# Optimization experiments

Measured on AMD Instinct MI355X. Metric: run time of the kernel, lower is better.

Reference implementation:

```python
import jax, jax.numpy as jnp
import numpy as np


def conv2d(x, w, b, pad):
    # x: [B,Cin,H,W], w: [Cout,Cin,kh,kw]
    y = jax.lax.conv_general_dilated(
        x, w, window_strides=(1, 1), padding=[(pad, pad), (pad, pad)],
        dimension_numbers=('NCHW', 'OIHW', 'NCHW'))
    return y + b[None, :, None, None]


def setup_inputs() -> dict:
    key = jax.random.key(0)
    ks = jax.random.split(key, 11)
    B, C, H, W = 4, 128, 64, 64
    Cc, Hc, Wc = 256, 32, 32
    s = 0.05
    return {
        'sr_feat': jax.random.normal(ks[0], (B, C, H, W), jnp.float32),
        'context_feat': jax.random.normal(ks[1], (B, Cc, Hc, Wc), jnp.float32),
        'Wq': jax.random.normal(ks[2], (C, C, 1, 1), jnp.float32) * s,
        'bq': jax.random.normal(ks[3], (C,), jnp.float32) * s,
        'Wk': jax.random.normal(ks[4], (C, Cc, 1, 1), jnp.float32) * s,
        'bk': jax.random.normal(ks[5], (C,), jnp.float32) * s,
        'Wv': jax.random.normal(ks[6], (C, Cc, 1, 1), jnp.float32) * s,
        'bv': jax.random.normal(ks[7], (C,), jnp.float32) * s,
        'Wp': jax.random.normal(ks[8], (C, C, 3, 3), jnp.float32) * s,
        'bp': jax.random.normal(ks[9], (C,), jnp.float32) * s,
        'gamma': jax.random.normal(ks[10], (1,), jnp.float32) * s,
    }


def reference(sr_feat, context_feat, Wq, bq, Wk, bk, Wv, bv, Wp, bp, gamma):
    B, C, H, W = sr_feat.shape
    Cc = context_feat.shape[1]
    # bilinear upsample (half-pixel centers == align_corners=False)
    ctx = jax.image.resize(context_feat, (B, Cc, H, W), method='bilinear')
    q = conv2d(sr_feat, Wq, bq, 0).reshape(B, C, H * W)   # [B,C,N]
    k = conv2d(ctx, Wk, bk, 0).reshape(B, C, H * W)       # [B,C,N]
    v = conv2d(ctx, Wv, bv, 0).reshape(B, C, H * W)       # [B,C,N]
    # attn[b,n,m] = softmax_m( sum_c q[b,c,n] * k[b,c,m] )
    attn = jax.nn.softmax(jnp.einsum('bcn,bcm->bnm', q, k), axis=-1)
    # out[b,c,n] = sum_m v[b,c,m] * attn[b,n,m]
    out = jnp.einsum('bcm,bnm->bcn', v, attn).reshape(B, C, H, W)
    return sr_feat + gamma[0] * conv2d(out, Wp, bp, 1)
```

## Files before the change

### kernel.cpp

```cpp
#include <hip/hip_runtime.h>
#include <math.h>

#define NB 4
#define C  128
#define CCH 256
#define HH 64
#define WW 64
#define NN 4096
#define HC 32
#define WC 32
#define PP 66
#define LOG2E 1.44269504088896f
#define NSPLIT 4

typedef unsigned short u16;
typedef unsigned int uint32;
typedef short s16x8 __attribute__((ext_vector_type(8)));
typedef float f32x4 __attribute__((ext_vector_type(4)));
typedef float f32x16 __attribute__((ext_vector_type(16)));

#if __has_builtin(__builtin_amdgcn_exp2f)
#define EXP2(x) __builtin_amdgcn_exp2f(x)
#else
#define EXP2(x) __expf((x) * 0.69314718056f)
#endif

__device__ __forceinline__ u16 f2bf(float f) {
    uint32 u = __float_as_uint(f);
    u += 0x7fffu + ((u >> 16) & 1u);
    return (u16)(u >> 16);
}
__device__ __forceinline__ float bf2f(u16 h) {
    return __uint_as_float((uint32)h << 16);
}

__global__ __launch_bounds__(256) void prep_all(const float* __restrict__ ctx,
                                                const float* __restrict__ sr,
                                                const float* __restrict__ Wq,
                                                const float* __restrict__ Wk,
                                                const float* __restrict__ Wv,
                                                const float* __restrict__ Wp,
                                                u16* __restrict__ ctx_t,
                                                u16* __restrict__ sr_t,
                                                u16* __restrict__ wbf,
                                                u16* __restrict__ wt,
                                                uint4* __restrict__ att_z) {
    __shared__ float smem[2 * 32 * 130];
    int blk = blockIdx.x;
    int tid = threadIdx.x;

    if (blk < 512) {
        float (*ls)[32][130] = (float(*)[32][130])smem;
        int y = blk & 63;
        int cch = (blk >> 6) & 1;
        int b = blk >> 7;
        float sy = y * 0.5f - 0.25f;
        int y0 = (int)floorf(sy);
        float wy = sy - (float)y0;
        int y0c = y0 < 0 ? 0 : y0;
        int y1c = (y0 + 1 > HC - 1) ? HC - 1 : y0 + 1;
#pragma unroll
        for (int t = 0; t < 4; t++) {
            int CI = t * 256 + tid;
            int cc = CI >> 3, xq = CI & 7;
            const float* s = ctx + (size_t)(b * CCH + cch * 128 + cc) * (HC * WC);
            float4 v0 = *(const float4*)(s + y0c * WC + xq * 4);
            float4 v1 = *(const float4*)(s + y1c * WC + xq * 4);
            ls[0][xq * 4 + 0][cc] = v0.x; ls[0][xq * 4 + 1][cc] = v0.y;
            ls[0][xq * 4 + 2][cc] = v0.z; ls[0][xq * 4 + 3][cc] = v0.w;
            ls[1][xq * 4 + 0][cc] = v1.x; ls[1][xq * 4 + 1][cc] = v1.y;
            ls[1][xq * 4 + 2][cc] = v1.z; ls[1][xq * 4 + 3][cc] = v1.w;
        }
        __syncthreads();
        int occ = tid & 127, xh = tid >> 7;
        u16* ob = ctx_t + ((size_t)b * NN + (size_t)y * 64) * CCH + cch * 128 + occ;
        float wy1 = 1.f - wy;
#pragma unroll
        for (int xi = 0; xi < 32; xi++) {
            int x = xi * 2 + xh;
            float sx = x * 0.5f - 0.25f;
            int x0 = (int)floorf(sx);
            float wx = sx - (float)x0;
            int x0c = x0 < 0 ? 0 : x0;
            int x1c = (x0 + 1 > WC - 1) ? WC - 1 : x0 + 1;
            float v00 = ls[0][x0c][occ], v01 = ls[0][x1c][occ];
            float v10 = ls[1][x0c][occ], v11 = ls[1][x1c][occ];
            float val = wy1 * ((1.f - wx) * v00 + wx * v01)
                      + wy  * ((1.f - wx) * v10 + wx * v11);
            ob[(size_t)x * CCH] = f2bf(val);
        }
    } else if (blk < 1024) {
        float* ls = smem;
        int idx = blk - 512;
        int n0 = (idx & 63) * 64;
        int ci0 = ((idx >> 6) & 1) * 64;
        int b = idx >> 7;
        const float* inb = sr + ((size_t)b * C + ci0) * NN + n0;
#pragma unroll
        for (int L = 0; L < 4; L++) {
            int fc = tid + L * 256;
            int nc = fc & 15, ci = fc >> 4;
            float4 v = *(const float4*)(inb + (size_t)ci * NN + nc * 4);
            float* d = &ls[ci * 65 + nc * 4];
            d[0] = v.x; d[1] = v.y; d[2] = v.z; d[3] = v.w;
        }
        __syncthreads();
        u16* ob = sr_t + ((size_t)b * NN + n0) * C + ci0;
#pragma unroll
        for (int j = 0; j < 16; j++) {
            int o = tid + j * 256;
            int ci = o & 63, n = o >> 6;
            ob[(size_t)n * C + ci] = f2bf(ls[ci * 65 + n]);
        }
    } else if (blk < 1920) {
        int i = (blk - 1024) * 256 + tid;
        if (i < 81920) {
            float v;
            if (i < 16384) v = Wq[i] * LOG2E;
            else if (i < 49152) v = Wk[i - 16384];
            else v = Wv[i - 49152];
            wbf[i] = f2bf(v);
        } else {
            int idx = i - 81920;
            int ciin = idx & 31;
            int co = (idx >> 5) & 127;
            int cb = (idx >> 12) & 3;
            int pos = idx >> 14;
            int ky = pos / 3, kx = pos - ky * 3;
            int ci = cb * 32 + ciin;
            wt[idx] = f2bf(Wp[((size_t)(co * C + ci) * 3 + ky) * 3 + kx]);
        }
    } else {
        int i = (blk - 1920) * 256 + tid;
        if (i < 278784) att_z[i] = make_uint4(0, 0, 0, 0);
    }
}

__global__ __launch_bounds__(256) void proj_all(const u16* __restrict__ sr_t,
                                                const u16* __restrict__ ctx_t,
                                                const u16* __restrict__ wbf,
                                                const float* __restrict__ bq,
                                                const float* __restrict__ bk,
                                                const float* __restrict__ bv,
                                                u16* __restrict__ q_t,
                                                u16* __restrict__ k_t,
                                                u16* __restrict__ v_bf) {
    __shared__ u16 xs[128 * 64];
    __shared__ u16 wsm[128 * 64];
    int z = blockIdx.z;
    int b = blockIdx.y;
    int n0 = blockIdx.x * 128;
    int Cin = (z == 0) ? C : CCH;
    const u16* xb = (z == 0 ? sr_t : ctx_t) + (size_t)b * NN * Cin;
    const u16* wb = wbf + (z == 0 ? 0 : (z == 1 ? 16384 : 49152));
    const float* bias = (z == 0) ? bq : (z == 1 ? bk : bv);
    float bsc = (z == 0) ? LOG2E : 1.0f;
    bool vmode = (z == 2);

    int tid = threadIdx.x;
    int w = tid >> 6, lane = tid & 63, l31 = lane & 31, half = lane >> 5;
    int xh = w >> 1, wh = w & 1;

    f32x16 acc[2][2];
#pragma unroll
    for (int xt = 0; xt < 2; xt++)
#pragma unroll
        for (int wt2 = 0; wt2 < 2; wt2++)
#pragma unroll
            for (int i = 0; i < 16; i++) acc[xt][wt2][i] = 0.f;

    int nchunks = Cin >> 6;
    for (int c0i = 0; c0i < nchunks; c0i++) {
        int c0 = c0i * 64;
        __syncthreads();
#pragma unroll
        for (int t = 0; t < 4; t++) {
            int CI = t * 256 + tid;
            int row = CI >> 3, sl = CI & 7;
            int lc = sl ^ (row & 7);
            __builtin_amdgcn_global_load_lds(
                (const __attribute__((address_space(1))) void*)(xb + (size_t)(n0 + row) * Cin + c0 + lc * 8),
                (__attribute__((address_space(3))) void*)&xs[(size_t)CI * 8], 16, 0, 0);
        }
#pragma unroll
        for (int t = 0; t < 4; t++) {
            int CI = t * 256 + tid;
            int co = CI >> 3, sl = CI & 7;
            int lc = sl ^ (co & 7);
            __builtin_amdgcn_global_load_lds(
                (const __attribute__((address_space(1))) void*)(wb + (size_t)co * Cin + c0 + lc * 8),
                (__attribute__((address_space(3))) void*)&wsm[(size_t)CI * 8], 16, 0, 0);
        }
        __syncthreads();
#pragma unroll
        for (int kg = 0; kg < 4; kg++) {
            int pc = ((kg * 2 + half) ^ (l31 & 7)) * 8;
            s16x8 xf[2], wf2[2];
#pragma unroll
            for (int xt = 0; xt < 2; xt++)
                xf[xt] = *(const s16x8*)&xs[(xh * 64 + xt * 32 + l31) * 64 + pc];
#pragma unroll
            for (int wt2 = 0; wt2 < 2; wt2++)
                wf2[wt2] = *(const s16x8*)&wsm[(wh * 64 + wt2 * 32 + l31) * 64 + pc];
#pragma unroll
            for (int xt = 0; xt < 2; xt++)
#pragma unroll
                for (int wt2 = 0; wt2 < 2; wt2++) {
                    if (vmode)
                        acc[xt][wt2] = __builtin_amdgcn_mfma_f32_32x32x16_bf16(wf2[wt2], xf[xt], acc[xt][wt2], 0, 0, 0);
                    else
                        acc[xt][wt2] = __builtin_amdgcn_mfma_f32_32x32x16_bf16(xf[xt], wf2[wt2], acc[xt][wt2], 0, 0, 0);
                }
        }
    }

    if (!vmode) {
        u16* ot = (z == 0 ? q_t : k_t) + (size_t)b * NN * C;
        float bv2[2];
#pragma unroll
        for (int wt2 = 0; wt2 < 2; wt2++) bv2[wt2] = bias[wh * 64 + wt2 * 32 + l31] * bsc;
#pragma unroll
        for (int xt = 0; xt < 2; xt++)
#pragma unroll
            for (int r = 0; r < 16; r++) {
                int n = n0 + xh * 64 + xt * 32 + (r & 3) + 8 * (r >> 2) + 4 * half;
#pragma unroll
                for (int wt2 = 0; wt2 < 2; wt2++)
                    ot[(size_t)n * C + wh * 64 + wt2 * 32 + l31] = f2bf(acc[xt][wt2][r] + bv2[wt2]);
            }
    } else {
        u16* ov = v_bf + (size_t)b * C * NN;
#pragma unroll
        for (int wt2 = 0; wt2 < 2; wt2++)
#pragma unroll
            for (int r = 0; r < 16; r++) {
                int co = wh * 64 + wt2 * 32 + (r & 3) + 8 * (r >> 2) + 4 * half;
                float bvv = bias[co];
#pragma unroll
                for (int xt = 0; xt < 2; xt++) {
                    int n = n0 + xh * 64 + xt * 32 + l31;
                    ov[(size_t)co * NN + n] = f2bf(acc[xt][wt2][r] + bvv);
                }
            }
    }
}

__global__ __launch_bounds__(256) void flash_mfma(const u16* __restrict__ qt_p,
                                                  const u16* __restrict__ kt_p,
                                                  const u16* __restrict__ vt_p,
                                                  u16* __restrict__ part,
                                                  float* __restrict__ lpart) {
    __shared__ u16 ks[2][64 * 128];
    __shared__ u16 vs[2][128 * 64];

    int ib = blockIdx.x;
    int b = (ib & 7) >> 1;
    int rest = ((ib >> 3) << 1) | (ib & 1);
    int qtile = rest >> 2;
    int split = rest & 3;
    int n0 = qtile * 128;
    int tid = threadIdx.x;
    int w = tid >> 6, lane = tid & 63, l31 = lane & 31, half = lane >> 5;

    const u16* qtb = qt_p + (size_t)b * NN * C;
    const u16* ktb = kt_p + (size_t)b * NN * C;
    const u16* vtb = vt_p + (size_t)b * C * NN;

    auto stageK = [&](int buf, int m0) {
#pragma unroll
        for (int t = 0; t < 4; t++) {
            int CI = (w * 4 + t) * 64 + lane;
            int r = CI >> 4;
            int lc = (CI & 15) ^ (r & 15);
            __builtin_amdgcn_global_load_lds(
                (const __attribute__((address_space(1))) void*)(ktb + (size_t)(m0 + r) * C + lc * 8),
                (__attribute__((address_space(3))) void*)&ks[buf][(w * 4 + t) * 512], 16, 0, 0);
        }
    };
    auto stageV = [&](int buf, int m0) {
#pragma unroll
        for (int t = 0; t < 4; t++) {
            int CI = (w * 4 + t) * 64 + lane;
            int c = CI >> 3;
            int lc = (CI & 7) ^ (c & 7);
            __builtin_amdgcn_global_load_lds(
                (const __attribute__((address_space(1))) void*)(vtb + (size_t)c * NN + m0 + lc * 8),
                (__attribute__((address_space(3))) void*)&vs[buf][(w * 4 + t) * 512], 16, 0, 0);
        }
    };

    int qrow = n0 + w * 32 + l31;
    s16x8 qf[8];
#pragma unroll
    for (int kg = 0; kg < 8; kg++)
        qf[kg] = *(const s16x8*)(qtb + (size_t)qrow * C + kg * 16 + half * 8);

    int m_base = split * 1024;
    stageK(0, m_base);
    stageV(0, m_base);
    __syncthreads();

    f32x16 oacc[4];
#pragma unroll
    for (int mt = 0; mt < 4; mt++)
#pragma unroll
        for (int i = 0; i < 16; i++) oacc[mt][i] = 0.f;
    float lsum = 0.f;

    for (int it = 0; it < 16; it++) {
        int buf = it & 1;
        int m0 = m_base + it * 64;
        if (it < 15) {
            stageK(buf ^ 1, m0 + 64);
            stageV(buf ^ 1, m0 + 64);
        }
        const u16* ksb = &ks[buf][0];
        const u16* vsb = &vs[buf][0];

#pragma unroll
        for (int kmt = 0; kmt < 2; kmt++) {
            f32x16 st;
#pragma unroll
            for (int i = 0; i < 16; i++) st[i] = 0.f;
#pragma unroll
            for (int kg = 0; kg < 8; kg++) {
                int pc = ((kg * 2 + half) ^ (l31 & 15)) * 8;
                s16x8 kf = *(const s16x8*)&ksb[(kmt * 32 + l31) * 128 + pc];
                st = __builtin_amdgcn_mfma_f32_32x32x16_bf16(kf, qf[kg], st, 0, 0, 0);
            }
            uint32 A[4], B4[4];
#pragma unroll
            for (int rg = 0; rg < 4; rg++) {
                float e0 = EXP2(st[rg * 4 + 0]);
                float e1 = EXP2(st[rg * 4 + 1]);
                float e2 = EXP2(st[rg * 4 + 2]);
                float e3 = EXP2(st[rg * 4 + 3]);
                lsum += (e0 + e1) + (e2 + e3);
                A[rg]  = __builtin_amdgcn_perm(__float_as_uint(e1), __float_as_uint(e0), 0x07060302u);
                B4[rg] = __builtin_amdgcn_perm(__float_as_uint(e3), __float_as_uint(e2), 0x07060302u);
            }
#pragma unroll
            for (int s = 0; s < 2; s++) {
                uint32 sendA = half ? A[2 * s] : A[2 * s + 1];
                uint32 sendB = half ? B4[2 * s] : B4[2 * s + 1];
                uint32 rA = __shfl_xor(sendA, 32);
                uint32 rB = __shfl_xor(sendB, 32);
                uint32 oA = half ? A[2 * s + 1] : A[2 * s];
                uint32 oB = half ? B4[2 * s + 1] : B4[2 * s];
                union { uint32 u[4]; s16x8 v; } pu;
                pu.u[0] = half ? rA : oA;
                pu.u[1] = half ? rB : oB;
                pu.u[2] = half ? oA : rA;
                pu.u[3] = half ? oB : rB;
                s16x8 pf = pu.v;
                int kgp = kmt * 2 + s;
                int pcv = ((kgp * 2 + half) ^ (l31 & 7)) * 8;
#pragma unroll
                for (int mt = 0; mt < 4; mt++) {
                    s16x8 vf = *(const s16x8*)&vsb[(mt * 32 + l31) * 64 + pcv];
                    oacc[mt] = __builtin_amdgcn_mfma_f32_32x32x16_bf16(vf, pf, oacc[mt], 0, 0, 0);
                }
            }
        }
        __syncthreads();
    }

    float lt = lsum + __shfl_xor(lsum, 32);
    if (half == 0) lpart[(size_t)split * NB * NN + (size_t)b * NN + qrow] = lt;
    u16* pb = part + ((size_t)split * NB + b) * (size_t)C * NN;
#pragma unroll
    for (int mt = 0; mt < 4; mt++)
#pragma unroll
        for (int r = 0; r < 16; r++) {
            int c = mt * 32 + (r & 3) + 8 * (r >> 2) + 4 * half;
            pb[(size_t)c * NN + n0 + w * 32 + l31] = f2bf(oacc[mt][r]);
        }
}

__global__ __launch_bounds__(256) void flash_combine(const u16* __restrict__ part,
                                                     const float* __restrict__ lpart,
                                                     u16* __restrict__ att_t) {
    __shared__ u16 ts[128 * 66];
    __shared__ float linv[64];
    int b = blockIdx.y;
    int nt = blockIdx.x;
    int n0 = nt * 64;
    int tid = threadIdx.x;
    if (tid < 64) {
        float s = 0.f;
#pragma unroll
        for (int sp = 0; sp < NSPLIT; sp++)
            s += lpart[(size_t)sp * NB * NN + (size_t)b * NN + n0 + tid];
        linv[tid] = 1.0f / s;
    }
    __syncthreads();
#pragma unroll
    for (int j = 0; j < 32; j++) {
        int e = tid + j * 256;
        int n = e & 63, c = e >> 6;
        float o = 0.f;
#pragma unroll
        for (int sp = 0; sp < NSPLIT; sp++)
            o += bf2f(part[((size_t)sp * NB + b) * (size_t)C * NN + (size_t)c * NN + n0 + n]);
        ts[c * 66 + n] = f2bf(o * linv[n]);
    }
    __syncthreads();
    u16* ob = att_t + ((size_t)b * PP * PP + (size_t)(nt + 1) * PP + 1) * C;
#pragma unroll
    for (int j = 0; j < 32; j++) {
        int o = tid + j * 256;
        int c = o & 127, n = o >> 7;
        ob[(size_t)n * C + c] = ts[c * 66 + n];
    }
}

__global__ __launch_bounds__(256) void conv3x3_mfma(const u16* __restrict__ att_t,
                                                    const u16* __restrict__ wt,
                                                    const float* __restrict__ bp,
                                                    const float* __restrict__ sr,
                                                    const float* __restrict__ gamma,
                                                    float* __restrict__ out) {
    __shared__ u16 in_s[2][4 * 102 * 8];
    int ib = blockIdx.x;
    int b = (ib & 7) >> 1;
    int rr = ((ib >> 3) << 1) | (ib & 1);
    int y = rr >> 1;
    int x0 = (rr & 1) * 32;
    int tid = threadIdx.x;
    int w = tid >> 6, lane = tid & 63, l = tid & 15, quad = (tid >> 4) & 3;
    const u16* ab = att_t + (size_t)b * (PP * PP * C);

    auto stage = [&](int cib, int bufi) {
        u16* base = &in_s[bufi][w * 102 * 8];
        const u16* gsrc = ab + cib * 32 + w * 8;
#pragma unroll
        for (int t = 0; t < 2; t++) {
            int idx = t * 64 + lane;
            int r = idx / 34, xp = idx - r * 34;
            if (t == 0 || lane < 38)
                __builtin_amdgcn_global_load_lds(
                    (const __attribute__((address_space(1))) void*)(gsrc + (size_t)((y + r) * PP + x0 + xp) * C),
                    (__attribute__((address_space(3))) void*)(base + (size_t)t * 64 * 8), 16, 0, 0);
        }
    };

    f32x4 accr[2][2];
#pragma unroll
    for (int cf = 0; cf < 2; cf++)
#pragma unroll
        for (int nf = 0; nf < 2; nf++) accr[cf][nf] = (f32x4){0.f, 0.f, 0.f, 0.f};
    int cow = w * 32;

    stage(0, 0);
    __syncthreads();
#pragma unroll
    for (int cib = 0; cib < 4; cib++) {
        if (cib < 3) stage(cib + 1, (cib + 1) & 1);
        s16x8 wf[9][2];
#pragma unroll
        for (int pos = 0; pos < 9; pos++)
#pragma unroll
            for (int cf = 0; cf < 2; cf++)
                wf[pos][cf] = *(const s16x8*)&wt[((size_t)(pos * 4 + cib) * C + cow + cf * 16 + l) * 32 + quad * 8];
        const u16* bufc = &in_s[cib & 1][0];
#pragma unroll
        for (int ky = 0; ky < 3; ky++)
#pragma unroll
            for (int kx = 0; kx < 3; kx++) {
                int pos = ky * 3 + kx;
#pragma unroll
                for (int nf = 0; nf < 2; nf++) {
                    s16x8 inf = *(const s16x8*)&bufc[(quad * 102 + ky * 34 + nf * 16 + l + kx) * 8];
                    accr[0][nf] = __builtin_amdgcn_mfma_f32_16x16x32_bf16(wf[pos][0], inf, accr[0][nf], 0, 0, 0);
                    accr[1][nf] = __builtin_amdgcn_mfma_f32_16x16x32_bf16(wf[pos][1], inf, accr[1][nf], 0, 0, 0);
                }
            }
        __syncthreads();
    }

    float g = gamma[0];
    float* ob = out + (size_t)b * C * NN;
    const float* sb = sr + (size_t)b * C * NN;
#pragma unroll
    for (int cf = 0; cf < 2; cf++)
#pragma unroll
        for (int r = 0; r < 4; r++) {
            int co = cow + cf * 16 + quad * 4 + r;
            float bias = bp[co];
#pragma unroll
            for (int nf = 0; nf < 2; nf++) {
                size_t oo = (size_t)co * NN + y * 64 + x0 + nf * 16 + l;
                ob[oo] = sb[oo] + g * (accr[cf][nf][r] + bias);
            }
        }
}

extern "C" void kernel_launch(void* const* d_in, const int* in_sizes, int n_in,
                              void* d_out, int out_size, void* d_ws, size_t ws_size,
                              hipStream_t stream) {
    const float* sr    = (const float*)d_in[0];
    const float* ctx   = (const float*)d_in[1];
    const float* Wq    = (const float*)d_in[2];
    const float* bq    = (const float*)d_in[3];
    const float* Wk    = (const float*)d_in[4];
    const float* bk    = (const float*)d_in[5];
    const float* Wv    = (const float*)d_in[6];
    const float* bv    = (const float*)d_in[7];
    const float* Wp    = (const float*)d_in[8];
    const float* bp    = (const float*)d_in[9];
    const float* gamma = (const float*)d_in[10];
    float* out = (float*)d_out;

    char* wsb = (char*)d_ws;
    u16*   att_t  = (u16*)wsb;
    u16*   part   = (u16*)(wsb + (5u << 20));
    float* lpart  = (float*)(wsb + (21u << 20));
    u16*   ctx_t  = (u16*)(wsb + (22u << 20));
    u16*   sr_t   = (u16*)(wsb + (30u << 20));
    u16*   q_t    = (u16*)(wsb + (34u << 20));
    u16*   k_t    = (u16*)(wsb + (38u << 20));
    u16*   v_bf   = (u16*)(wsb + (42u << 20));
    u16*   wt     = (u16*)(wsb + (46u << 20));
    u16*   w_bf   = (u16*)(wsb + (46u << 20) + (512u << 10));

    prep_all<<<dim3(3009), 256, 0, stream>>>(ctx, sr, Wq, Wk, Wv, Wp,
                                             ctx_t, sr_t, w_bf, wt,
                                             (uint4*)att_t);
    proj_all<<<dim3(32, NB, 3), 256, 0, stream>>>(sr_t, ctx_t, w_bf, bq, bk, bv,
                                                  q_t, k_t, v_bf);
    flash_mfma<<<dim3(512), 256, 0, stream>>>(q_t, k_t, v_bf, part, lpart);
    flash_combine<<<dim3(64, NB), 256, 0, stream>>>(part, lpart, att_t);
    conv3x3_mfma<<<dim3(512), 256, 0, stream>>>(att_t, wt, bp, sr, gamma, out);
}
```

Baseline: 161.9 us.

## Project K/V at low resolution before bilinear upsampling

The K and V 1x1 convolutions are linear and commute with bilinear upsampling, so they now run on the 32x32 context instead of the upsampled 64x64 map. This cuts the projection FLOPs and the context transpose traffic by about 4x. A new upsample_kv kernel then expands the 128-channel K and V to full resolution. The cost is an extra kernel launch and slightly different bf16 rounding order.

```diff
diff --git a/kernel.cpp b/kernel.cpp
--- a/kernel.cpp
+++ b/kernel.cpp
@@ -7,6 +7,7 @@
 #define HH 64
 #define WW 64
 #define NN 4096
+#define NS 1024
 #define HC 32
 #define WC 32
 #define PP 66
@@ -34,64 +35,45 @@
     return __uint_as_float((uint32)h << 16);
 }
 
-__global__ __launch_bounds__(256) void prep_all(const float* __restrict__ ctx,
-                                                const float* __restrict__ sr,
-                                                const float* __restrict__ Wq,
-                                                const float* __restrict__ Wk,
-                                                const float* __restrict__ Wv,
-                                                const float* __restrict__ Wp,
-                                                u16* __restrict__ ctx_t,
-                                                u16* __restrict__ sr_t,
-                                                u16* __restrict__ wbf,
-                                                u16* __restrict__ wt,
-                                                uint4* __restrict__ att_z) {
-    __shared__ float smem[2 * 32 * 130];
+__global__ __launch_bounds__(256) void prep2(const float* __restrict__ ctx,
+                                             const float* __restrict__ sr,
+                                             const float* __restrict__ Wq,
+                                             const float* __restrict__ Wk,
+                                             const float* __restrict__ Wv,
+                                             const float* __restrict__ Wp,
+                                             u16* __restrict__ ctx_s,
+                                             u16* __restrict__ sr_t,
+                                             u16* __restrict__ wbf,
+                                             u16* __restrict__ wt,
+                                             uint4* __restrict__ att_z) {
+    __shared__ float ls[64 * 65];
     int blk = blockIdx.x;
     int tid = threadIdx.x;
 
-    if (blk < 512) {
-        float (*ls)[32][130] = (float(*)[32][130])smem;
-        int y = blk & 63;
-        int cch = (blk >> 6) & 1;
-        int b = blk >> 7;
-        float sy = y * 0.5f - 0.25f;
-        int y0 = (int)floorf(sy);
-        float wy = sy - (float)y0;
-        int y0c = y0 < 0 ? 0 : y0;
-        int y1c = (y0 + 1 > HC - 1) ? HC - 1 : y0 + 1;
-#pragma unroll
-        for (int t = 0; t < 4; t++) {
-            int CI = t * 256 + tid;
-            int cc = CI >> 3, xq = CI & 7;
-            const float* s = ctx + (size_t)(b * CCH + cch * 128 + cc) * (HC * WC);
-            float4 v0 = *(const float4*)(s + y0c * WC + xq * 4);
-            float4 v1 = *(const float4*)(s + y1c * WC + xq * 4);
-            ls[0][xq * 4 + 0][cc] = v0.x; ls[0][xq * 4 + 1][cc] = v0.y;
-            ls[0][xq * 4 + 2][cc] = v0.z; ls[0][xq * 4 + 3][cc] = v0.w;
-            ls[1][xq * 4 + 0][cc] = v1.x; ls[1][xq * 4 + 1][cc] = v1.y;
-            ls[1][xq * 4 + 2][cc] = v1.z; ls[1][xq * 4 + 3][cc] = v1.w;
+    if (blk < 256) {
+        int idx = blk;
+        int n0 = (idx & 15) * 64;
+        int ci0 = ((idx >> 4) & 3) * 64;
+        int b = idx >> 6;
+        const float* inb = ctx + ((size_t)b * CCH + ci0) * NS + n0;
+#pragma unroll
+        for (int L = 0; L < 4; L++) {
+            int fc = tid + L * 256;
+            int nc = fc & 15, ci = fc >> 4;
+            float4 v = *(const float4*)(inb + (size_t)ci * NS + nc * 4);
+            float* d = &ls[ci * 65 + nc * 4];
+            d[0] = v.x; d[1] = v.y; d[2] = v.z; d[3] = v.w;
         }
         __syncthreads();
-        int occ = tid & 127, xh = tid >> 7;
-        u16* ob = ctx_t + ((size_t)b * NN + (size_t)y * 64) * CCH + cch * 128 + occ;
-        float wy1 = 1.f - wy;
-#pragma unroll
-        for (int xi = 0; xi < 32; xi++) {
-            int x = xi * 2 + xh;
-            float sx = x * 0.5f - 0.25f;
-            int x0 = (int)floorf(sx);
-            float wx = sx - (float)x0;
-            int x0c = x0 < 0 ? 0 : x0;
-            int x1c = (x0 + 1 > WC - 1) ? WC - 1 : x0 + 1;
-            float v00 = ls[0][x0c][occ], v01 = ls[0][x1c][occ];
-            float v10 = ls[1][x0c][occ], v11 = ls[1][x1c][occ];
-            float val = wy1 * ((1.f - wx) * v00 + wx * v01)
-                      + wy  * ((1.f - wx) * v10 + wx * v11);
-            ob[(size_t)x * CCH] = f2bf(val);
-        }
-    } else if (blk < 1024) {
-        float* ls = smem;
-        int idx = blk - 512;
+        u16* ob = ctx_s + ((size_t)b * NS + n0) * CCH + ci0;
+#pragma unroll
+        for (int j = 0; j < 16; j++) {
+            int o = tid + j * 256;
+            int ci = o & 63, n = o >> 6;
+            ob[(size_t)n * CCH + ci] = f2bf(ls[ci * 65 + n]);
+        }
+    } else if (blk < 768) {
+        int idx = blk - 256;
         int n0 = (idx & 63) * 64;
         int ci0 = ((idx >> 6) & 1) * 64;
         int b = idx >> 7;
@@ -112,8 +94,8 @@
             int ci = o & 63, n = o >> 6;
             ob[(size_t)n * C + ci] = f2bf(ls[ci * 65 + n]);
         }
-    } else if (blk < 1920) {
-        int i = (blk - 1024) * 256 + tid;
+    } else if (blk < 1664) {
+        int i = (blk - 768) * 256 + tid;
         if (i < 81920) {
             float v;
             if (i < 16384) v = Wq[i] * LOG2E;
@@ -131,94 +113,80 @@
             wt[idx] = f2bf(Wp[((size_t)(co * C + ci) * 3 + ky) * 3 + kx]);
         }
     } else {
-        int i = (blk - 1920) * 256 + tid;
+        int i = (blk - 1664) * 256 + tid;
         if (i < 278784) att_z[i] = make_uint4(0, 0, 0, 0);
     }
 }
 
-__global__ __launch_bounds__(256) void proj_all(const u16* __restrict__ sr_t,
-                                                const u16* __restrict__ ctx_t,
-                                                const u16* __restrict__ wbf,
-                                                const float* __restrict__ bq,
-                                                const float* __restrict__ bk,
-                                                const float* __restrict__ bv,
-                                                u16* __restrict__ q_t,
-                                                u16* __restrict__ k_t,
-                                                u16* __restrict__ v_bf) {
+__global__ __launch_bounds__(256) void proj_all2(const u16* __restrict__ sr_t,
+                                                 const u16* __restrict__ ctx_s,
+                                                 const u16* __restrict__ wbf,
+                                                 const float* __restrict__ bq,
+                                                 const float* __restrict__ bk,
+                                                 const float* __restrict__ bv,
+                                                 u16* __restrict__ q_t,
+                                                 u16* __restrict__ k_s,
+                                                 u16* __restrict__ v_s) {
     __shared__ u16 xs[128 * 64];
-    __shared__ u16 wsm[128 * 64];
-    int z = blockIdx.z;
+    __shared__ u16 wsm[2][128 * 64];
     int b = blockIdx.y;
-    int n0 = blockIdx.x * 128;
-    int Cin = (z == 0) ? C : CCH;
-    const u16* xb = (z == 0 ? sr_t : ctx_t) + (size_t)b * NN * Cin;
-    const u16* wb = wbf + (z == 0 ? 0 : (z == 1 ? 16384 : 49152));
-    const float* bias = (z == 0) ? bq : (z == 1 ? bk : bv);
-    float bsc = (z == 0) ? LOG2E : 1.0f;
-    bool vmode = (z == 2);
-
     int tid = threadIdx.x;
     int w = tid >> 6, lane = tid & 63, l31 = lane & 31, half = lane >> 5;
     int xh = w >> 1, wh = w & 1;
 
-    f32x16 acc[2][2];
-#pragma unroll
-    for (int xt = 0; xt < 2; xt++)
-#pragma unroll
-        for (int wt2 = 0; wt2 < 2; wt2++)
-#pragma unroll
-            for (int i = 0; i < 16; i++) acc[xt][wt2][i] = 0.f;
-
-    int nchunks = Cin >> 6;
-    for (int c0i = 0; c0i < nchunks; c0i++) {
-        int c0 = c0i * 64;
-        __syncthreads();
-#pragma unroll
-        for (int t = 0; t < 4; t++) {
-            int CI = t * 256 + tid;
-            int row = CI >> 3, sl = CI & 7;
-            int lc = sl ^ (row & 7);
-            __builtin_amdgcn_global_load_lds(
-                (const __attribute__((address_space(1))) void*)(xb + (size_t)(n0 + row) * Cin + c0 + lc * 8),
-                (__attribute__((address_space(3))) void*)&xs[(size_t)CI * 8], 16, 0, 0);
-        }
-#pragma unroll
-        for (int t = 0; t < 4; t++) {
-            int CI = t * 256 + tid;
-            int co = CI >> 3, sl = CI & 7;
-            int lc = sl ^ (co & 7);
-            __builtin_amdgcn_global_load_lds(
-                (const __attribute__((address_space(1))) void*)(wb + (size_t)co * Cin + c0 + lc * 8),
-                (__attribute__((address_space(3))) void*)&wsm[(size_t)CI * 8], 16, 0, 0);
-        }
-        __syncthreads();
-#pragma unroll
-        for (int kg = 0; kg < 4; kg++) {
-            int pc = ((kg * 2 + half) ^ (l31 & 7)) * 8;
-            s16x8 xf[2], wf2[2];
-#pragma unroll
-            for (int xt = 0; xt < 2; xt++)
-                xf[xt] = *(const s16x8*)&xs[(xh * 64 + xt * 32 + l31) * 64 + pc];
+    if (blockIdx.x < 32) {
+        int n0 = blockIdx.x * 128;
+        const u16* xb = sr_t + (size_t)b * NN * C;
+        f32x16 acc[2][2];
+#pragma unroll
+        for (int xt = 0; xt < 2; xt++)
 #pragma unroll
             for (int wt2 = 0; wt2 < 2; wt2++)
-                wf2[wt2] = *(const s16x8*)&wsm[(wh * 64 + wt2 * 32 + l31) * 64 + pc];
-#pragma unroll
-            for (int xt = 0; xt < 2; xt++)
-#pragma unroll
-                for (int wt2 = 0; wt2 < 2; wt2++) {
-                    if (vmode)
-                        acc[xt][wt2] = __builtin_amdgcn_mfma_f32_32x32x16_bf16(wf2[wt2], xf[xt], acc[xt][wt2], 0, 0, 0);
-                    else
+#pragma unroll
+                for (int i = 0; i < 16; i++) acc[xt][wt2][i] = 0.f;
+        for (int c0i = 0; c0i < 2; c0i++) {
+            int c0 = c0i * 64;
+            __syncthreads();
+#pragma unroll
+            for (int t = 0; t < 4; t++) {
+                int CI = t * 256 + tid;
+                int row = CI >> 3, sl = CI & 7;
+                int lc = sl ^ (row & 7);
+                __builtin_amdgcn_global_load_lds(
+                    (const __attribute__((address_space(1))) void*)(xb + (size_t)(n0 + row) * C + c0 + lc * 8),
+                    (__attribute__((address_space(3))) void*)&xs[(size_t)CI * 8], 16, 0, 0);
+            }
+#pragma unroll
+            for (int t = 0; t < 4; t++) {
+                int CI = t * 256 + tid;
+                int co = CI >> 3, sl = CI & 7;
+                int lc = sl ^ (co & 7);
+                __builtin_amdgcn_global_load_lds(
+                    (const __attribute__((address_space(1))) void*)(wbf + (size_t)co * C + c0 + lc * 8),
+                    (__attribute__((address_space(3))) void*)&wsm[0][(size_t)CI * 8], 16, 0, 0);
+            }
+            __syncthreads();
+#pragma unroll
+            for (int kg = 0; kg < 4; kg++) {
+                int pc = ((kg * 2 + half) ^ (l31 & 7)) * 8;
+                s16x8 xf[2], wf2[2];
+#pragma unroll
+                for (int xt = 0; xt < 2; xt++)
+                    xf[xt] = *(const s16x8*)&xs[(xh * 64 + xt * 32 + l31) * 64 + pc];
+#pragma unroll
+                for (int wt2 = 0; wt2 < 2; wt2++)
+                    wf2[wt2] = *(const s16x8*)&wsm[0][(wh * 64 + wt2 * 32 + l31) * 64 + pc];
+#pragma unroll
+                for (int xt = 0; xt < 2; xt++)
+#pragma unroll
+                    for (int wt2 = 0; wt2 < 2; wt2++)
                         acc[xt][wt2] = __builtin_amdgcn_mfma_f32_32x32x16_bf16(xf[xt], wf2[wt2], acc[xt][wt2], 0, 0, 0);
-                }
-        }
-    }
-
-    if (!vmode) {
-        u16* ot = (z == 0 ? q_t : k_t) + (size_t)b * NN * C;
+            }
+        }
+        u16* ot = q_t + (size_t)b * NN * C;
         float bv2[2];
 #pragma unroll
-        for (int wt2 = 0; wt2 < 2; wt2++) bv2[wt2] = bias[wh * 64 + wt2 * 32 + l31] * bsc;
+        for (int wt2 = 0; wt2 < 2; wt2++) bv2[wt2] = bq[wh * 64 + wt2 * 32 + l31] * LOG2E;
 #pragma unroll
         for (int xt = 0; xt < 2; xt++)
 #pragma unroll
@@ -229,19 +197,142 @@
                     ot[(size_t)n * C + wh * 64 + wt2 * 32 + l31] = f2bf(acc[xt][wt2][r] + bv2[wt2]);
             }
     } else {
-        u16* ov = v_bf + (size_t)b * C * NN;
+        int n0 = (blockIdx.x - 32) * 64;
+        const u16* xb = ctx_s + (size_t)b * NS * CCH;
+        const u16* wkb = wbf + 16384;
+        const u16* wvb = wbf + 49152;
+        f32x16 acck[2], accv[2];
+#pragma unroll
+        for (int wt2 = 0; wt2 < 2; wt2++)
+#pragma unroll
+            for (int i = 0; i < 16; i++) { acck[wt2][i] = 0.f; accv[wt2][i] = 0.f; }
+        for (int c0i = 0; c0i < 4; c0i++) {
+            int c0 = c0i * 64;
+            __syncthreads();
+#pragma unroll
+            for (int t = 0; t < 2; t++) {
+                int CI = t * 256 + tid;
+                int row = CI >> 3, sl = CI & 7;
+                int lc = sl ^ (row & 7);
+                __builtin_amdgcn_global_load_lds(
+                    (const __attribute__((address_space(1))) void*)(xb + (size_t)(n0 + row) * CCH + c0 + lc * 8),
+                    (__attribute__((address_space(3))) void*)&xs[(size_t)CI * 8], 16, 0, 0);
+            }
+#pragma unroll
+            for (int t = 0; t < 4; t++) {
+                int CI = t * 256 + tid;
+                int co = CI >> 3, sl = CI & 7;
+                int lc = sl ^ (co & 7);
+                __builtin_amdgcn_global_load_lds(
+                    (const __attribute__((address_space(1))) void*)(wkb + (size_t)co * CCH + c0 + lc * 8),
+                    (__attribute__((address_space(3))) void*)&wsm[0][(size_t)CI * 8], 16, 0, 0);
+            }
+#pragma unroll
+            for (int t = 0; t < 4; t++) {
+                int CI = t * 256 + tid;
+                int co = CI >> 3, sl = CI & 7;
+                int lc = sl ^ (co & 7);
+                __builtin_amdgcn_global_load_lds(
+                    (const __attribute__((address_space(1))) void*)(wvb + (size_t)co * CCH + c0 + lc * 8),
+                    (__attribute__((address_space(3))) void*)&wsm[1][(size_t)CI * 8], 16, 0, 0);
+            }
+            __syncthreads();
+#pragma unroll
+            for (int kg = 0; kg < 4; kg++) {
+                int pc = ((kg * 2 + half) ^ (l31 & 7)) * 8;
+                s16x8 xf = *(const s16x8*)&xs[(xh * 32 + l31) * 64 + pc];
+                s16x8 wfk[2], wfv[2];
+#pragma unroll
+                for (int wt2 = 0; wt2 < 2; wt2++) {
+                    wfk[wt2] = *(const s16x8*)&wsm[0][(wh * 64 + wt2 * 32 + l31) * 64 + pc];
+                    wfv[wt2] = *(const s16x8*)&wsm[1][(wh * 64 + wt2 * 32 + l31) * 64 + pc];
+                }
+#pragma unroll
+                for (int wt2 = 0; wt2 < 2; wt2++) {
+                    acck[wt2] = __builtin_amdgcn_mfma_f32_32x32x16_bf16(xf, wfk[wt2], acck[wt2], 0, 0, 0);
+                    accv[wt2] = __builtin_amdgcn_mfma_f32_32x32x16_bf16(wfv[wt2], xf, accv[wt2], 0, 0, 0);
+                }
+            }
+        }
+        u16* ok = k_s + (size_t)b * NS * C;
+#pragma unroll
+        for (int wt2 = 0; wt2 < 2; wt2++) {
+            float bvk = bk[wh * 64 + wt2 * 32 + l31];
+#pragma unroll
+            for (int r = 0; r < 16; r++) {
+                int n = n0 + xh * 32 + (r & 3) + 8 * (r >> 2) + 4 * half;
+                ok[(size_t)n * C + wh * 64 + wt2 * 32 + l31] = f2bf(acck[wt2][r] + bvk);
+            }
+        }
+        u16* ov = v_s + (size_t)b * C * NS;
 #pragma unroll
         for (int wt2 = 0; wt2 < 2; wt2++)
 #pragma unroll
             for (int r = 0; r < 16; r++) {
                 int co = wh * 64 + wt2 * 32 + (r & 3) + 8 * (r >> 2) + 4 * half;
-                float bvv = bias[co];
-#pragma unroll
-                for (int xt = 0; xt < 2; xt++) {
-                    int n = n0 + xh * 64 + xt * 32 + l31;
-                    ov[(size_t)co * NN + n] = f2bf(acc[xt][wt2][r] + bvv);
-                }
-            }
+                ov[(size_t)co * NS + n0 + xh * 32 + l31] = f2bf(accv[wt2][r] + bv[co]);
+            }
+    }
+}
+
+__global__ __launch_bounds__(256) void upsample_kv(const u16* __restrict__ k_s,
+                                                   const u16* __restrict__ v_s,
+                                                   u16* __restrict__ k_t,
+                                                   u16* __restrict__ v_bf) {
+    __shared__ u16 lsv[NS];
+    int blk = blockIdx.x;
+    int tid = threadIdx.x;
+    if (blk < 256) {
+        int y = blk & 63, b = blk >> 6;
+        float sy = y * 0.5f - 0.25f;
+        int y0 = (int)floorf(sy);
+        float wy = sy - (float)y0;
+        int y0c = y0 < 0 ? 0 : y0;
+        int y1c = (y0 + 1 > HC - 1) ? HC - 1 : y0 + 1;
+        int occ = tid & 127, xh = tid >> 7;
+        const u16* kb = k_s + (size_t)b * NS * C;
+        u16* ob = k_t + ((size_t)b * NN + (size_t)y * 64) * C + occ;
+        float wy1 = 1.f - wy;
+#pragma unroll
+        for (int xi = 0; xi < 32; xi++) {
+            int x = xi * 2 + xh;
+            float sx = x * 0.5f - 0.25f;
+            int x0 = (int)floorf(sx);
+            float wx = sx - (float)x0;
+            int x0c = x0 < 0 ? 0 : x0;
+            int x1c = (x0 + 1 > WC - 1) ? WC - 1 : x0 + 1;
+            float v00 = bf2f(kb[(size_t)(y0c * WC + x0c) * C + occ]);
+            float v01 = bf2f(kb[(size_t)(y0c * WC + x1c) * C + occ]);
+            float v10 = bf2f(kb[(size_t)(y1c * WC + x0c) * C + occ]);
+            float v11 = bf2f(kb[(size_t)(y1c * WC + x1c) * C + occ]);
+            float val = wy1 * ((1.f - wx) * v00 + wx * v01)
+                      + wy  * ((1.f - wx) * v10 + wx * v11);
+            ob[(size_t)x * C] = f2bf(val);
+        }
+    } else {
+        int idx = blk - 256;
+        int c = idx & 127, b = idx >> 7;
+        const u16* vp = v_s + ((size_t)b * C + c) * NS;
+        if (tid < 128) *(uint4*)&lsv[tid * 8] = *(const uint4*)(vp + tid * 8);
+        __syncthreads();
+        u16* ob = v_bf + ((size_t)b * C + c) * NN;
+#pragma unroll
+        for (int j = 0; j < 16; j++) {
+            int n = tid + j * 256;
+            int y = n >> 6, x = n & 63;
+            float sy = y * 0.5f - 0.25f;
+            float sx = x * 0.5f - 0.25f;
+            int y0 = (int)floorf(sy), x0 = (int)floorf(sx);
+            float wy = sy - (float)y0, wx = sx - (float)x0;
+            int y0c = y0 < 0 ? 0 : y0;
+            int y1c = (y0 + 1 > HC - 1) ? HC - 1 : y0 + 1;
+            int x0c = x0 < 0 ? 0 : x0;
+            int x1c = (x0 + 1 > WC - 1) ? WC - 1 : x0 + 1;
+            float v00 = bf2f(lsv[y0c * WC + x0c]), v01 = bf2f(lsv[y0c * WC + x1c]);
+            float v10 = bf2f(lsv[y1c * WC + x0c]), v11 = bf2f(lsv[y1c * WC + x1c]);
+            ob[n] = f2bf((1.f - wy) * ((1.f - wx) * v00 + wx * v01)
+                       +        wy  * ((1.f - wx) * v10 + wx * v11));
+        }
     }
 }
 
@@ -515,19 +606,21 @@
     u16*   att_t  = (u16*)wsb;
     u16*   part   = (u16*)(wsb + (5u << 20));
     float* lpart  = (float*)(wsb + (21u << 20));
-    u16*   ctx_t  = (u16*)(wsb + (22u << 20));
-    u16*   sr_t   = (u16*)(wsb + (30u << 20));
-    u16*   q_t    = (u16*)(wsb + (34u << 20));
-    u16*   k_t    = (u16*)(wsb + (38u << 20));
-    u16*   v_bf   = (u16*)(wsb + (42u << 20));
-    u16*   wt     = (u16*)(wsb + (46u << 20));
-    u16*   w_bf   = (u16*)(wsb + (46u << 20) + (512u << 10));
-
-    prep_all<<<dim3(3009), 256, 0, stream>>>(ctx, sr, Wq, Wk, Wv, Wp,
-                                             ctx_t, sr_t, w_bf, wt,
-                                             (uint4*)att_t);
-    proj_all<<<dim3(32, NB, 3), 256, 0, stream>>>(sr_t, ctx_t, w_bf, bq, bk, bv,
-                                                  q_t, k_t, v_bf);
+    u16*   ctx_s  = (u16*)(wsb + (22u << 20));
+    u16*   sr_t   = (u16*)(wsb + (25u << 20));
+    u16*   q_t    = (u16*)(wsb + (29u << 20));
+    u16*   k_s    = (u16*)(wsb + (33u << 20));
+    u16*   v_s    = (u16*)(wsb + (34u << 20));
+    u16*   k_t    = (u16*)(wsb + (35u << 20));
+    u16*   v_bf   = (u16*)(wsb + (39u << 20));
+    u16*   wt     = (u16*)(wsb + (43u << 20));
+    u16*   w_bf   = (u16*)(wsb + (43u << 20) + (512u << 10));
+
+    prep2<<<dim3(2753), 256, 0, stream>>>(ctx, sr, Wq, Wk, Wv, Wp,
+                                          ctx_s, sr_t, w_bf, wt, (uint4*)att_t);
+    proj_all2<<<dim3(48, NB), 256, 0, stream>>>(sr_t, ctx_s, w_bf, bq, bk, bv,
+                                                q_t, k_s, v_s);
+    upsample_kv<<<dim3(768), 256, 0, stream>>>(k_s, v_s, k_t, v_bf);
     flash_mfma<<<dim3(512), 256, 0, stream>>>(q_t, k_t, v_bf, part, lpart);
     flash_combine<<<dim3(64, NB), 256, 0, stream>>>(part, lpart, att_t);
     conv3x3_mfma<<<dim3(512), 256, 0, stream>>>(att_t, wt, bp, sr, gamma, out);
```

Result: no change. 161.1 us (-0.5%).
